# Kernel tuning notes

Measured on AMD Instinct MI355X. Metric: run time of the kernel, lower is better.

The kernel has to match this reference:

```python
import jax, jax.numpy as jnp
import numpy as np

B, L, D = 4, 512, 128
PAD_TOKEN = 0
LN_EPS = 1e-5


def setup_inputs() -> dict:
    key = jax.random.key(0)
    ks = jax.random.split(key, 8)
    x = jax.random.normal(ks[0], (B, L, L, D), dtype=jnp.float32)
    coord = jax.random.normal(ks[1], (B, L, 3), dtype=jnp.float32)
    nodes = jax.random.randint(ks[2], (B, L), 0, 30, dtype=jnp.int64)
    # params (torch defaults: LN gamma=1, beta=0; Linear kaiming-uniform-ish -> use scaled normals)
    ln_g = jnp.ones((D,), dtype=jnp.float32)
    ln_b = jnp.zeros((D,), dtype=jnp.float32)
    s = 1.0 / np.sqrt(D)
    w1 = jax.random.uniform(ks[3], (D, D), jnp.float32, -s, s)
    b1 = jax.random.uniform(ks[4], (D,), jnp.float32, -s, s)
    w2 = jax.random.uniform(ks[5], (D, 1), jnp.float32, -s, s)
    b2 = jax.random.uniform(ks[6], (1,), jnp.float32, -s, s)
    return {"x": x, "coord": coord, "nodes": nodes,
            "ln_g": ln_g, "ln_b": ln_b, "w1": w1, "b1": b1, "w2": w2, "b2": b2}


def reference(x, coord, nodes, ln_g, ln_b, w1, b1, w2, b2):
    # LayerNorm over last dim D
    mu = jnp.mean(x, axis=-1, keepdims=True)
    var = jnp.mean(jnp.square(x - mu), axis=-1, keepdims=True)
    h = (x - mu) * jax.lax.rsqrt(var + LN_EPS) * ln_g + ln_b  # [B,L,L,D]
    pad = (nodes == PAD_TOKEN)  # [B,L] bool
    # masked_fill with mask [B,1,L,1]: zero columns j that are padding
    h = jnp.where(pad[:, None, :, None], 0.0, h)
    not_pad = 1.0 - pad.astype(x.dtype)  # [B,L]
    atom_num = jnp.sum(not_pad, axis=1).reshape(-1, 1, 1, 1)  # [B,1,1,1]
    # proj: Linear -> GELU(exact) -> Linear
    hidden = jax.nn.gelu(jnp.einsum('blmd,de->blme', h, w1) + b1, approximate=False)
    attn_probs = jnp.einsum('blmd,de->blme', hidden, w2) + b2  # [B,L,L,1]
    delta_pos = coord[:, None, :, :] - coord[:, :, None, :]  # [B,L,L,3]
    coord_update = delta_pos / atom_num * attn_probs
    pair_mask = not_pad[:, None, :] * not_pad[:, :, None]  # [B,L,L]
    coord_update = coord_update * pair_mask[..., None]
    coord_update = jnp.sum(coord_update, axis=2)  # [B,L,3]
    return coord + coord_update
```

## Files before the change

kernel.cpp:

```cpp
#include <hip/hip_runtime.h>
#include <hip/hip_bf16.h>
#include <math.h>

#define NB 4
#define NL 512
#define ND 128
#define KSTR 136

typedef __attribute__((ext_vector_type(8))) short bf16x8;
typedef __attribute__((ext_vector_type(4))) float f32x4;

__device__ __forceinline__ short f2bf(float f) {
  union { float f; unsigned u; } un; un.f = f;
  unsigned r = un.u + 0x7FFFu + ((un.u >> 16) & 1u);
  return (short)(r >> 16);
}

__device__ __forceinline__ float gelu_exact(float h) {
  const float z = 0.70710678118f * h;
  const float az = fabsf(z);
  const float t = __builtin_amdgcn_rcpf(fmaf(0.3275911f, az, 1.0f));
  float p = fmaf(1.061405429f, t, -1.453152027f);
  p = fmaf(p, t, 1.421413741f);
  p = fmaf(p, t, -0.284496736f);
  p = fmaf(p, t, 0.254829592f);
  p = p * t;
  const float ex = exp2f(az * az * -1.4426950408f);
  const float e = fmaf(-p, ex, 1.0f);
  const float se = copysignf(e, z);
  const float hh = 0.5f * h;
  return fmaf(hh, se, hh);
}

__global__ void unimol_prep(const float* __restrict__ w1, const float* __restrict__ ln_g,
                            const float* __restrict__ ln_b, const float* __restrict__ b1,
                            const int* __restrict__ nodes,
                            short* __restrict__ w1f, float* __restrict__ b1p,
                            float* __restrict__ npad, float* __restrict__ inva) {
  const int tid = threadIdx.x;
  for (int idx = tid; idx < ND * ND; idx += 256) {
    const int k = idx >> 7, n = idx & (ND - 1);
    w1f[n * ND + k] = f2bf(w1[idx] * ln_g[k]);
  }
  if (tid < ND) {
    float s = b1[tid];
    for (int k = 0; k < ND; ++k) s = fmaf(ln_b[k], w1[k * ND + tid], s);
    b1p[tid] = s;
  }
  for (int j = tid; j < NB * NL; j += 256) npad[j] = (nodes[j] != 0) ? 1.0f : 0.0f;
  const int wv = tid >> 6, lane = tid & 63;
  if (wv < NB) {
    float s = 0.f;
    for (int j = lane; j < NL; j += 64) s += (nodes[wv * NL + j] != 0) ? 1.0f : 0.0f;
    #pragma unroll
    for (int m = 1; m <= 32; m <<= 1) s += __shfl_xor(s, m);
    if (lane == 0) inva[wv] = 1.0f / s;
  }
}

__global__ __launch_bounds__(256, 2) void unimol_coord_head(
    const float* __restrict__ x, const float* __restrict__ coord,
    const int* __restrict__ nodes, const float* __restrict__ w2,
    const float* __restrict__ b2,
    const short* __restrict__ w1f, const float* __restrict__ b1pw,
    const float* __restrict__ npadw, const float* __restrict__ invw,
    float* __restrict__ out)
{
  __shared__ __align__(16) short w1T[ND * KSTR];
  __shared__ float b1p[ND];
  __shared__ float notpad[NL];
  __shared__ float coord_s[NL * 3];
  __shared__ float red[16];

  const int blk = blockIdx.x;
  const int bb = blk >> 9;
  const int lrow = blk & (NL - 1);
  const int tid = threadIdx.x;

  if (nodes[bb * NL + lrow] == 0) {
    if (tid < 3) out[(bb * NL + lrow) * 3 + tid] = coord[(bb * NL + lrow) * 3 + tid];
    return;
  }

  for (int t = tid; t < (ND * ND) / 8; t += 256) {
    const int row = t >> 4, cg = (t & 15) << 3;
    *reinterpret_cast<bf16x8*>(&w1T[row * KSTR + cg]) =
        *reinterpret_cast<const bf16x8*>(&w1f[row * ND + cg]);
  }
  if (tid < ND) b1p[tid] = b1pw[tid];
  for (int j = tid; j < NL; j += 256) notpad[j] = npadw[bb * NL + j];
  for (int j = tid; j < NL * 3; j += 256) coord_s[j] = coord[bb * (NL * 3) + j];
  __syncthreads();

  const int lane = tid & 63;
  const int wv = tid >> 6;
  const int c = lane & 15;
  const int g = lane >> 4;
  float b1r[8], w2r[8];
  #pragma unroll
  for (int nt = 0; nt < 8; ++nt) { b1r[nt] = b1p[16 * nt + c]; w2r[nt] = w2[16 * nt + c]; }
  const float b2c = b2[0] * (1.0f / 16.0f);

  float s0 = 0.f, sx = 0.f, sy = 0.f, sz = 0.f;
  const size_t xbase = (size_t)(bb * NL + lrow) * (NL * ND);

  for (int it = 0; it < 8; ++it) {
    const int mbase = (it << 6) + (wv << 4);
    const float* xr = x + xbase + (size_t)(mbase + c) * ND + 8 * g;
    f32x4 xv[8];
    #pragma unroll
    for (int ks = 0; ks < 4; ++ks) {
      xv[2 * ks]     = *reinterpret_cast<const f32x4*>(xr + 32 * ks);
      xv[2 * ks + 1] = *reinterpret_cast<const f32x4*>(xr + 32 * ks + 4);
    }
    float sum = 0.f, sq = 0.f;
    #pragma unroll
    for (int q = 0; q < 8; ++q) {
      #pragma unroll
      for (int j = 0; j < 4; ++j) { const float e = xv[q][j]; sum += e; sq = fmaf(e, e, sq); }
    }
    sum += __shfl_xor(sum, 16); sum += __shfl_xor(sum, 32);
    sq  += __shfl_xor(sq, 16);  sq  += __shfl_xor(sq, 32);
    const float mu = sum * (1.0f / ND);
    const float rs = rsqrtf(fmaf(-mu, mu, sq * (1.0f / ND)) + 1e-5f);
    const float nmr = -mu * rs;

    bf16x8 af[4];
    #pragma unroll
    for (int ks = 0; ks < 4; ++ks) {
      #pragma unroll
      for (int j = 0; j < 8; ++j) {
        const float e = (j < 4) ? xv[2 * ks][j] : xv[2 * ks + 1][j - 4];
        af[ks][j] = f2bf(fmaf(e, rs, nmr));
      }
    }

    f32x4 acc[8];
    #pragma unroll
    for (int nt = 0; nt < 8; ++nt) acc[nt] = (f32x4){0.f, 0.f, 0.f, 0.f};
    #pragma unroll
    for (int ks = 0; ks < 4; ++ks) {
      const int koff = 8 * g + 32 * ks;
      #pragma unroll
      for (int nt = 0; nt < 8; ++nt) {
        const bf16x8 bf = *reinterpret_cast<const bf16x8*>(&w1T[(16 * nt + c) * KSTR + koff]);
        acc[nt] = __builtin_amdgcn_mfma_f32_16x16x32_bf16(af[ks], bf, acc[nt], 0, 0, 0);
      }
    }

    float p[4] = {0.f, 0.f, 0.f, 0.f};
    #pragma unroll
    for (int nt = 0; nt < 8; ++nt) {
      #pragma unroll
      for (int i = 0; i < 4; ++i) {
        const float h = acc[nt][i] + b1r[nt];
        p[i] = fmaf(gelu_exact(h), w2r[nt], p[i]);
      }
    }
    #pragma unroll
    for (int i = 0; i < 4; ++i) {
      const int m = mbase + 4 * g + i;
      const float a = (p[i] + b2c) * notpad[m];
      s0 += a;
      sx = fmaf(a, coord_s[3 * m + 0], sx);
      sy = fmaf(a, coord_s[3 * m + 1], sy);
      sz = fmaf(a, coord_s[3 * m + 2], sz);
    }
  }

  #pragma unroll
  for (int m = 1; m <= 32; m <<= 1) {
    s0 += __shfl_xor(s0, m); sx += __shfl_xor(sx, m);
    sy += __shfl_xor(sy, m); sz += __shfl_xor(sz, m);
  }
  if (lane == 0) {
    red[wv * 4 + 0] = s0; red[wv * 4 + 1] = sx;
    red[wv * 4 + 2] = sy; red[wv * 4 + 3] = sz;
  }
  __syncthreads();
  if (tid == 0) {
    const float S0 = red[0] + red[4] + red[8] + red[12];
    const float SX = red[1] + red[5] + red[9] + red[13];
    const float SY = red[2] + red[6] + red[10] + red[14];
    const float SZ = red[3] + red[7] + red[11] + red[15];
    const float ia = invw[bb];
    const float cx = coord_s[3 * lrow + 0], cy = coord_s[3 * lrow + 1], cz = coord_s[3 * lrow + 2];
    float* o = out + (bb * NL + lrow) * 3;
    o[0] = cx + (SX - S0 * cx) * ia;
    o[1] = cy + (SY - S0 * cy) * ia;
    o[2] = cz + (SZ - S0 * cz) * ia;
  }
}

extern "C" void kernel_launch(void* const* d_in, const int* in_sizes, int n_in,
                              void* d_out, int out_size, void* d_ws, size_t ws_size,
                              hipStream_t stream) {
  const float* x     = (const float*)d_in[0];
  const float* coord = (const float*)d_in[1];
  const int*   nodes = (const int*)d_in[2];
  const float* ln_g  = (const float*)d_in[3];
  const float* ln_b  = (const float*)d_in[4];
  const float* w1    = (const float*)d_in[5];
  const float* b1    = (const float*)d_in[6];
  const float* w2    = (const float*)d_in[7];
  const float* b2    = (const float*)d_in[8];
  float* out = (float*)d_out;

  short* w1f  = (short*)d_ws;
  float* b1p  = (float*)((char*)d_ws + 32768);
  float* npad = (float*)((char*)d_ws + 33280);
  float* inva = (float*)((char*)d_ws + 41472);
  hipLaunchKernelGGL(unimol_prep, dim3(1), dim3(256), 0, stream,
                     w1, ln_g, ln_b, b1, nodes, w1f, b1p, npad, inva);
  hipLaunchKernelGGL(unimol_coord_head, dim3(NB * NL), dim3(256), 0, stream,
                     x, coord, nodes, w2, b2, w1f, b1p, npad, inva, out);
}
```

Before: 191.1 us.

## Double-buffer x row loads and pack bf16 conversions in coord head loop

The per-iteration loop is unrolled by two and split into LOADX/CONSUME macros with two register buffers. The next 16-row slice of x is issued before the LayerNorm, MFMA and GELU work on the current slice, so global load latency overlaps with compute. The bf16 conversion of the normalized activations also switches from the hand-written scalar rounding to the packed __float22bfloat162_rn intrinsic. The extra 32 floats of buffer per thread raise register pressure, which could cause spills or cut occupancy under the 256x2 launch bounds.

Measured after the change: 326.4 us. 1.71x slower.

```diff
diff --git a/kernel.cpp b/kernel.cpp
--- a/kernel.cpp
+++ b/kernel.cpp
@@ -58,6 +58,87 @@
   }
 }
 
+#define LOADX(buf, itv)                                                         \
+  do {                                                                          \
+    const float* xr_ = x + xbase + (size_t)((((itv) << 6) + (wv << 4)) + c) * ND + 8 * g; \
+    _Pragma("unroll")                                                           \
+    for (int ks_ = 0; ks_ < 4; ++ks_) {                                         \
+      buf[2 * ks_]     = *reinterpret_cast<const f32x4*>(xr_ + 32 * ks_);       \
+      buf[2 * ks_ + 1] = *reinterpret_cast<const f32x4*>(xr_ + 32 * ks_ + 4);   \
+    }                                                                           \
+  } while (0)
+
+#define CONSUME(buf, itv)                                                       \
+  do {                                                                          \
+    const int mbase_ = ((itv) << 6) + (wv << 4);                                \
+    float sum_ = 0.f, sq_ = 0.f;                                                \
+    _Pragma("unroll")                                                           \
+    for (int q_ = 0; q_ < 8; ++q_) {                                            \
+      _Pragma("unroll")                                                         \
+      for (int j_ = 0; j_ < 4; ++j_) {                                          \
+        const float e_ = buf[q_][j_]; sum_ += e_; sq_ = fmaf(e_, e_, sq_);      \
+      }                                                                         \
+    }                                                                           \
+    sum_ += __shfl_xor(sum_, 16); sum_ += __shfl_xor(sum_, 32);                 \
+    sq_  += __shfl_xor(sq_, 16);  sq_  += __shfl_xor(sq_, 32);                  \
+    const float mu_ = sum_ * (1.0f / ND);                                       \
+    const float rs_ = rsqrtf(fmaf(-mu_, mu_, sq_ * (1.0f / ND)) + 1e-5f);       \
+    const float nmr_ = -mu_ * rs_;                                              \
+    bf16x8 af_[4];                                                              \
+    _Pragma("unroll")                                                           \
+    for (int ks_ = 0; ks_ < 4; ++ks_) {                                         \
+      union { bf16x8 v; __hip_bfloat162 h[4]; } u_;                            \
+      _Pragma("unroll")                                                         \
+      for (int p_ = 0; p_ < 2; ++p_) {                                          \
+        float2 f0_, f1_;                                                        \
+        f0_.x = fmaf(buf[2 * ks_ + p_ * 0][0], rs_, nmr_);                      \
+        f0_.y = fmaf(buf[2 * ks_][1], rs_, nmr_);                               \
+        f1_.x = fmaf(buf[2 * ks_][2], rs_, nmr_);                               \
+        f1_.y = fmaf(buf[2 * ks_][3], rs_, nmr_);                               \
+        if (p_ == 0) { u_.h[0] = __float22bfloat162_rn(f0_); u_.h[1] = __float22bfloat162_rn(f1_); } \
+        else {                                                                  \
+          float2 g0_, g1_;                                                      \
+          g0_.x = fmaf(buf[2 * ks_ + 1][0], rs_, nmr_);                         \
+          g0_.y = fmaf(buf[2 * ks_ + 1][1], rs_, nmr_);                         \
+          g1_.x = fmaf(buf[2 * ks_ + 1][2], rs_, nmr_);                         \
+          g1_.y = fmaf(buf[2 * ks_ + 1][3], rs_, nmr_);                         \
+          u_.h[2] = __float22bfloat162_rn(g0_); u_.h[3] = __float22bfloat162_rn(g1_); \
+        }                                                                       \
+      }                                                                         \
+      af_[ks_] = u_.v;                                                          \
+    }                                                                           \
+    f32x4 acc_[8];                                                              \
+    _Pragma("unroll")                                                           \
+    for (int nt_ = 0; nt_ < 8; ++nt_) acc_[nt_] = (f32x4){0.f, 0.f, 0.f, 0.f};  \
+    _Pragma("unroll")                                                           \
+    for (int ks_ = 0; ks_ < 4; ++ks_) {                                         \
+      const int koff_ = 8 * g + 32 * ks_;                                       \
+      _Pragma("unroll")                                                         \
+      for (int nt_ = 0; nt_ < 8; ++nt_) {                                       \
+        const bf16x8 bf_ = *reinterpret_cast<const bf16x8*>(&w1T[(16 * nt_ + c) * KSTR + koff_]); \
+        acc_[nt_] = __builtin_amdgcn_mfma_f32_16x16x32_bf16(af_[ks_], bf_, acc_[nt_], 0, 0, 0); \
+      }                                                                         \
+    }                                                                           \
+    float p_[4] = {0.f, 0.f, 0.f, 0.f};                                         \
+    _Pragma("unroll")                                                           \
+    for (int nt_ = 0; nt_ < 8; ++nt_) {                                         \
+      _Pragma("unroll")                                                         \
+      for (int i_ = 0; i_ < 4; ++i_) {                                          \
+        const float h_ = acc_[nt_][i_] + b1r[nt_];                              \
+        p_[i_] = fmaf(gelu_exact(h_), w2r[nt_], p_[i_]);                        \
+      }                                                                         \
+    }                                                                           \
+    _Pragma("unroll")                                                           \
+    for (int i_ = 0; i_ < 4; ++i_) {                                            \
+      const int m_ = mbase_ + 4 * g + i_;                                       \
+      const float a_ = (p_[i_] + b2c) * notpad[m_];                             \
+      s0 += a_;                                                                 \
+      sx = fmaf(a_, coord_s[3 * m_ + 0], sx);                                   \
+      sy = fmaf(a_, coord_s[3 * m_ + 1], sy);                                   \
+      sz = fmaf(a_, coord_s[3 * m_ + 2], sz);                                   \
+    }                                                                           \
+  } while (0)
+
 __global__ __launch_bounds__(256, 2) void unimol_coord_head(
     const float* __restrict__ x, const float* __restrict__ coord,
     const int* __restrict__ nodes, const float* __restrict__ w2,
@@ -104,68 +185,14 @@
   float s0 = 0.f, sx = 0.f, sy = 0.f, sz = 0.f;
   const size_t xbase = (size_t)(bb * NL + lrow) * (NL * ND);
 
-  for (int it = 0; it < 8; ++it) {
-    const int mbase = (it << 6) + (wv << 4);
-    const float* xr = x + xbase + (size_t)(mbase + c) * ND + 8 * g;
-    f32x4 xv[8];
-    #pragma unroll
-    for (int ks = 0; ks < 4; ++ks) {
-      xv[2 * ks]     = *reinterpret_cast<const f32x4*>(xr + 32 * ks);
-      xv[2 * ks + 1] = *reinterpret_cast<const f32x4*>(xr + 32 * ks + 4);
-    }
-    float sum = 0.f, sq = 0.f;
-    #pragma unroll
-    for (int q = 0; q < 8; ++q) {
-      #pragma unroll
-      for (int j = 0; j < 4; ++j) { const float e = xv[q][j]; sum += e; sq = fmaf(e, e, sq); }
-    }
-    sum += __shfl_xor(sum, 16); sum += __shfl_xor(sum, 32);
-    sq  += __shfl_xor(sq, 16);  sq  += __shfl_xor(sq, 32);
-    const float mu = sum * (1.0f / ND);
-    const float rs = rsqrtf(fmaf(-mu, mu, sq * (1.0f / ND)) + 1e-5f);
-    const float nmr = -mu * rs;
-
-    bf16x8 af[4];
-    #pragma unroll
-    for (int ks = 0; ks < 4; ++ks) {
-      #pragma unroll
-      for (int j = 0; j < 8; ++j) {
-        const float e = (j < 4) ? xv[2 * ks][j] : xv[2 * ks + 1][j - 4];
-        af[ks][j] = f2bf(fmaf(e, rs, nmr));
-      }
-    }
-
-    f32x4 acc[8];
-    #pragma unroll
-    for (int nt = 0; nt < 8; ++nt) acc[nt] = (f32x4){0.f, 0.f, 0.f, 0.f};
-    #pragma unroll
-    for (int ks = 0; ks < 4; ++ks) {
-      const int koff = 8 * g + 32 * ks;
-      #pragma unroll
-      for (int nt = 0; nt < 8; ++nt) {
-        const bf16x8 bf = *reinterpret_cast<const bf16x8*>(&w1T[(16 * nt + c) * KSTR + koff]);
-        acc[nt] = __builtin_amdgcn_mfma_f32_16x16x32_bf16(af[ks], bf, acc[nt], 0, 0, 0);
-      }
-    }
-
-    float p[4] = {0.f, 0.f, 0.f, 0.f};
-    #pragma unroll
-    for (int nt = 0; nt < 8; ++nt) {
-      #pragma unroll
-      for (int i = 0; i < 4; ++i) {
-        const float h = acc[nt][i] + b1r[nt];
-        p[i] = fmaf(gelu_exact(h), w2r[nt], p[i]);
-      }
-    }
-    #pragma unroll
-    for (int i = 0; i < 4; ++i) {
-      const int m = mbase + 4 * g + i;
-      const float a = (p[i] + b2c) * notpad[m];
-      s0 += a;
-      sx = fmaf(a, coord_s[3 * m + 0], sx);
-      sy = fmaf(a, coord_s[3 * m + 1], sy);
-      sz = fmaf(a, coord_s[3 * m + 2], sz);
-    }
+  f32x4 xvA[8], xvB[8];
+  LOADX(xvA, 0);
+  #pragma unroll 1
+  for (int it2 = 0; it2 < 4; ++it2) {
+    LOADX(xvB, 2 * it2 + 1);
+    CONSUME(xvA, 2 * it2);
+    if (it2 < 3) LOADX(xvA, 2 * it2 + 2);
+    CONSUME(xvB, 2 * it2 + 1);
   }
 
   #pragma unroll
```
